# Kernel optimization log

Hardware: AMD Instinct MI355X
Metric: run time of the kernel (lower is better)

## Reference

```python
import jax, jax.numpy as jnp
import numpy as np

B, S, D, H = 4, 1024, 512, 8
DH = D // H  # 64 head dim; max_len == S for the masked (preceding_only) skew path


def setup_inputs() -> dict:
    key = jax.random.key(0)
    ks = jax.random.split(key, 8)
    queries = jax.random.normal(ks[0], (B, S, D), jnp.float32)
    keys_ = jax.random.normal(ks[1], (B, S, D), jnp.float32)
    values = jax.random.normal(ks[2], (B, S, D), jnp.float32)
    Wq = jax.random.normal(ks[3], (D, D), jnp.float32) * 0.03
    Wk = jax.random.normal(ks[4], (D, D), jnp.float32) * 0.03
    Wv = jax.random.normal(ks[5], (D, D), jnp.float32) * 0.03
    Wo = jax.random.normal(ks[6], (D, D), jnp.float32) * 0.03
    rel_emb = jax.random.normal(ks[7], (H, DH, S), jnp.float32) * 0.03  # preceding_only -> len == max_len
    i = jnp.arange(S)
    mask = jnp.where(i[None, :] > i[:, None], -1e9, 0.0).astype(jnp.float32)[None, None]  # [1,1,S,S] causal
    return {"queries": queries, "keys": keys_, "values": values, "mask": mask,
            "Wq": Wq, "Wk": Wk, "Wv": Wv, "Wo": Wo, "rel_emb": rel_emb}


def _skewed_rel_bias(q, rel_emb):
    # q: [B,H,S,DH], rel_emb: [H,DH,L] with L == max_len == S
    b, h, s, _ = q.shape
    L = rel_emb.shape[-1]
    qe = jnp.einsum('bhsd,hdl->bhsl', q, rel_emb)  # [B,H,S,L]
    # _qe_masking: keep qe[..., i, j] where j >= L-1-i
    lengths = (L - 1) - jnp.arange(s)
    keep = (jnp.arange(L)[None, :] >= lengths[:, None]).astype(qe.dtype)
    qe = qe * keep
    # skew: pad one column on the left, fold into [B,H,L+1,S], drop first row
    qe = jnp.pad(qe, ((0, 0), (0, 0), (0, 0), (1, 0)))
    qe = qe.reshape(b, h, L + 1, s)[:, :, 1:, :]  # [B,H,L,S]
    return qe


def reference(queries, keys, values, mask, Wq, Wk, Wv, Wo, rel_emb):
    b, s, _ = queries.shape
    h, dh, _ = rel_emb.shape
    scale = dh ** -0.5

    def split(x):  # [B,S,H*DH] -> [B,H,S,DH]
        return x.reshape(b, s, h, dh).transpose(0, 2, 1, 3)

    q = split(queries @ Wq)
    k = split(keys @ Wk)
    v = split(values @ Wv)

    logits = jnp.einsum('bhsd,bhtd->bhst', q, k)
    logits = logits + _skewed_rel_bias(q, rel_emb)
    logits = (logits + mask[:, :, :s, :s]) * scale  # original scales after adding mask
    weights = jax.nn.softmax(logits, axis=-1)
    ctx = jnp.einsum('bhst,bhtd->bhsd', weights, v)
    ctx = ctx.transpose(0, 2, 1, 3).reshape(b, s, h * dh)
    return ctx @ Wo
```

## Files before the change

kernel.cpp:

```cpp
#include <hip/hip_runtime.h>
#include <hip/hip_bf16.h>

#define SB 4
#define SS 1024
#define SD 512
#define SH 8
#define SDH 64

typedef short bf16x8 __attribute__((ext_vector_type(8)));
typedef float f32x4 __attribute__((ext_vector_type(4)));

#define MFMA(a, b, c) __builtin_amdgcn_mfma_f32_16x16x32_bf16(a, b, c, 0, 0, 0)

__device__ __forceinline__ void load_lds16(const void* g, void* l) {
  __builtin_amdgcn_global_load_lds(
      (__attribute__((address_space(1))) void*)(const_cast<void*>(g)),
      (__attribute__((address_space(3))) void*)(l), 16, 0, 0);
}

__global__ __launch_bounds__(256) void k_prep(
    const float* __restrict__ q, const float* __restrict__ k, const float* __restrict__ v,
    const float* __restrict__ Wq, const float* __restrict__ Wk, const float* __restrict__ Wv,
    const float* __restrict__ Wo, const float* __restrict__ rel,
    __hip_bfloat16* __restrict__ Xq, __hip_bfloat16* __restrict__ Xk,
    __hip_bfloat16* __restrict__ Xv, __hip_bfloat16* __restrict__ Wqt,
    __hip_bfloat16* __restrict__ Wkt, __hip_bfloat16* __restrict__ Wvt,
    __hip_bfloat16* __restrict__ Wot, __hip_bfloat16* __restrict__ relT) {
  __shared__ float tile[32][33];
  const int y = blockIdx.y, x = blockIdx.x, t = threadIdx.x;
  if (y < 3) {
    const float2* in = (const float2*)(y == 0 ? q : y == 1 ? k : v);
    __hip_bfloat162* out = (__hip_bfloat162*)(y == 0 ? Xq : y == 1 ? Xk : Xv);
    const int n2 = SB * SS * SD / 2;
    int i = x * 256 + t, st = 512 * 256;
    for (; i < n2; i += st) out[i] = __float22bfloat162_rn(in[i]);
    return;
  }
  int tx = t & 31, ty = t >> 5;
  if (y < 5) {
    int which = (y - 3) * 2 + (x >> 8), idx = x & 255;
    const float* ip = which == 0 ? Wq : which == 1 ? Wk : which == 2 ? Wv : Wo;
    __hip_bfloat16* op = which == 0 ? Wqt : which == 1 ? Wkt : which == 2 ? Wvt : Wot;
    int c0 = (idx & 15) * 32, r0 = (idx >> 4) * 32;
    for (int rr = ty; rr < 32; rr += 8) tile[rr][tx] = ip[(size_t)(r0 + rr) * SD + c0 + tx];
    __syncthreads();
    for (int cc = ty; cc < 32; cc += 8)
      op[(size_t)(c0 + cc) * SD + r0 + tx] = __float2bfloat16(tile[tx][cc]);
    return;
  }
  int hd = x >> 6, idx = x & 63;
  int c0 = (idx >> 1) * 32, r0 = (idx & 1) * 32;
  const float* ip = rel + (size_t)hd * SDH * SS;
  __hip_bfloat16* op = relT + (size_t)hd * SDH * SS;
  for (int rr = ty; rr < 32; rr += 8) tile[rr][tx] = ip[(size_t)(r0 + rr) * SS + c0 + tx];
  __syncthreads();
  for (int cc = ty; cc < 32; cc += 8)
    op[(size_t)(c0 + cc) * SDH + r0 + tx] = __float2bfloat16(tile[tx][cc]);
}

__device__ __forceinline__ void gemm_core(const __hip_bfloat16* __restrict__ A,
                                          const __hip_bfloat16* __restrict__ Bt,
                                          void* __restrict__ Cout, int mode) {
  __shared__ __hip_bfloat16 As[128 * 64];
  __shared__ __hip_bfloat16 Bs[64 * 64];
  const int t = threadIdx.x, w = t >> 6, lane = t & 63;
  const int quad = lane >> 4, l16 = lane & 15;
  const int m0 = blockIdx.y * 128, n0 = blockIdx.x * 64;
  const int wm = (w >> 1) * 64, wn = (w & 1) * 32;
  f32x4 zero4 = {0.0f, 0.0f, 0.0f, 0.0f};
  f32x4 acc[4][2];
#pragma unroll
  for (int mi = 0; mi < 4; ++mi)
#pragma unroll
    for (int nj = 0; nj < 2; ++nj) acc[mi][nj] = zero4;

  for (int kt = 0; kt < SD; kt += 64) {
#pragma unroll
    for (int c = 0; c < 4; ++c) {
      int ofs = c * 256 + t;
      int row = ofs >> 3, col = (ofs & 7) ^ (row & 7);
      load_lds16(A + (size_t)(m0 + row) * SD + kt + col * 8,
                 (char*)As + (size_t)(c * 256 + w * 64) * 16);
    }
#pragma unroll
    for (int c = 0; c < 2; ++c) {
      int ofs = c * 256 + t;
      int row = ofs >> 3, col = (ofs & 7) ^ (row & 7);
      load_lds16(Bt + (size_t)(n0 + row) * SD + kt + col * 8,
                 (char*)Bs + (size_t)(c * 256 + w * 64) * 16);
    }
    __syncthreads();
    bf16x8 af[4][2], bfr[2][2];
#pragma unroll
    for (int mi = 0; mi < 4; ++mi) {
      int row = wm + mi * 16 + l16;
#pragma unroll
      for (int ks = 0; ks < 2; ++ks)
        af[mi][ks] = *(const bf16x8*)((const char*)As + row * 128 +
                                      ((ks * 4 + quad) ^ (row & 7)) * 16);
    }
#pragma unroll
    for (int nj = 0; nj < 2; ++nj) {
      int row = wn + nj * 16 + l16;
#pragma unroll
      for (int ks = 0; ks < 2; ++ks)
        bfr[nj][ks] = *(const bf16x8*)((const char*)Bs + row * 128 +
                                       ((ks * 4 + quad) ^ (row & 7)) * 16);
    }
#pragma unroll
    for (int mi = 0; mi < 4; ++mi)
#pragma unroll
      for (int nj = 0; nj < 2; ++nj) {
        acc[mi][nj] = MFMA(af[mi][0], bfr[nj][0], acc[mi][nj]);
        acc[mi][nj] = MFMA(af[mi][1], bfr[nj][1], acc[mi][nj]);
      }
    __syncthreads();
  }
#pragma unroll
  for (int mi = 0; mi < 4; ++mi)
#pragma unroll
    for (int nj = 0; nj < 2; ++nj)
#pragma unroll
      for (int r = 0; r < 4; ++r) {
        int m = m0 + wm + mi * 16 + quad * 4 + r;
        int n = n0 + wn + nj * 16 + l16;
        float v = acc[mi][nj][r];
        if (mode == 2) {
          ((float*)Cout)[(size_t)m * SD + n] = v;
        } else {
          int b = m >> 10, s = m & 1023, hh = n >> 6, dh = n & 63;
          __hip_bfloat16 bv = __float2bfloat16(v);
          if (mode == 0)
            ((__hip_bfloat16*)Cout)[((size_t)(b * SH + hh) * SS + s) * SDH + dh] = bv;
          else
            ((__hip_bfloat16*)Cout)[((size_t)(b * SH + hh) * SDH + dh) * SS + s] = bv;
        }
      }
}

__global__ __launch_bounds__(256) void k_gemm_qkv(
    const __hip_bfloat16* __restrict__ Xq, const __hip_bfloat16* __restrict__ Xk,
    const __hip_bfloat16* __restrict__ Xv, const __hip_bfloat16* __restrict__ Wqt,
    const __hip_bfloat16* __restrict__ Wkt, const __hip_bfloat16* __restrict__ Wvt,
    __hip_bfloat16* __restrict__ Qb, __hip_bfloat16* __restrict__ Kb,
    __hip_bfloat16* __restrict__ Vt) {
  int z = blockIdx.z;
  const __hip_bfloat16* A = z == 0 ? Xq : z == 1 ? Xk : Xv;
  const __hip_bfloat16* Bt = z == 0 ? Wqt : z == 1 ? Wkt : Wvt;
  void* C = z == 0 ? (void*)Qb : z == 1 ? (void*)Kb : (void*)Vt;
  gemm_core(A, Bt, C, z == 2 ? 1 : 0);
}

__global__ __launch_bounds__(256) void k_gemm_o(const __hip_bfloat16* __restrict__ CTX,
                                                const __hip_bfloat16* __restrict__ Wot,
                                                float* __restrict__ Out) {
  gemm_core(CTX, Wot, Out, 2);
}

__device__ const int TTm[40] = {0,1,2,3,4,4,5,5,6,6,7,7,8,8,8,9,9,9,10,10,10,11,11,11,
                                12,12,12,12,13,13,13,13,14,14,14,14,15,15,15,15};
__device__ const int CCm[40] = {0,0,0,0,0,1,0,1,0,1,0,1,0,1,2,0,1,2,0,1,2,0,1,2,
                                0,1,2,3,0,1,2,3,0,1,2,3,0,1,2,3};

__global__ __launch_bounds__(256) void k_flash(const __hip_bfloat16* __restrict__ Qb,
                                               const __hip_bfloat16* __restrict__ Kb,
                                               const __hip_bfloat16* __restrict__ Vt,
                                               const __hip_bfloat16* __restrict__ relT,
                                               float* __restrict__ Opart,
                                               float* __restrict__ lpart) {
  __shared__ __hip_bfloat16 Klds[64 * 64];
  __shared__ __hip_bfloat16 Vlds[64 * 64];
  __shared__ __hip_bfloat16 REs[128 * 64];
  __shared__ __hip_bfloat16 QEP[64 * 136];
  const int t = threadIdx.x, w = t >> 6, lane = t & 63;
  const int quad = lane >> 4, l16 = lane & 15;
  const int idx = blockIdx.x, bh = blockIdx.y, h = bh & 7;
  const int tI = TTm[idx], c = CCm[idx];
  const int i0 = tI * 64;
  const int rem = tI + 1 - c * 4;
  const int nt = rem < 4 ? rem : 4;
  const size_t qbase = (size_t)bh * SS * SDH;
  const __hip_bfloat16* Rp = relT + (size_t)h * SS * SDH;

  const int qrow = i0 + w * 16 + l16;
  bf16x8 qf0 = *(const bf16x8*)(Qb + qbase + (size_t)qrow * SDH + quad * 8);
  bf16x8 qf1 = *(const bf16x8*)(Qb + qbase + (size_t)qrow * SDH + 32 + quad * 8);

  f32x4 zero4 = {0.0f, 0.0f, 0.0f, 0.0f};
  f32x4 acc_o[4];
#pragma unroll
  for (int dt = 0; dt < 4; ++dt) acc_o[dt] = zero4;
  float ls[4] = {0.0f, 0.0f, 0.0f, 0.0f};
  const int rloc = quad * 4;
  const int irow_base = i0 + w * 16 + rloc;

  for (int jt = 0; jt < nt; ++jt) {
    const int jtile = c * 4 + jt, j0 = jtile * 64;
    const int l0 = 960 - 64 * (tI - jtile);
#pragma unroll
    for (int cc = 0; cc < 2; ++cc) {
      int ofs = cc * 256 + t;
      int row = ofs >> 3, col = (ofs & 7) ^ (row & 7);
      load_lds16(Kb + qbase + (size_t)(j0 + row) * SDH + col * 8,
                 (char*)Klds + (size_t)(cc * 256 + w * 64) * 16);
      load_lds16(Vt + (size_t)bh * SDH * SS + (size_t)row * SS + j0 + col * 8,
                 (char*)Vlds + (size_t)(cc * 256 + w * 64) * 16);
    }
#pragma unroll
    for (int cc = 0; cc < 4; ++cc) {
      int ofs = cc * 256 + t;
      int row = ofs >> 3, col = (ofs & 7) ^ (row & 7);
      int lr = l0 + row;
      if (lr > 1023) lr = 1023;
      load_lds16(Rp + (size_t)lr * SDH + col * 8,
                 (char*)REs + (size_t)(cc * 256 + w * 64) * 16);
    }
    __syncthreads();

    f32x4 s[4];
#pragma unroll
    for (int nj = 0; nj < 4; ++nj) {
      int row = nj * 16 + l16;
      bf16x8 b0 = *(const bf16x8*)((const char*)Klds + row * 128 + (quad ^ (row & 7)) * 16);
      bf16x8 b1 = *(const bf16x8*)((const char*)Klds + row * 128 + ((4 + quad) ^ (row & 7)) * 16);
      f32x4 z = zero4;
      z = MFMA(qf0, b0, z);
      z = MFMA(qf1, b1, z);
      s[nj] = z;
    }
#pragma unroll
    for (int nc = 0; nc < 8; ++nc) {
      int row = nc * 16 + l16;
      bf16x8 b0 = *(const bf16x8*)((const char*)REs + row * 128 + (quad ^ (row & 7)) * 16);
      bf16x8 b1 = *(const bf16x8*)((const char*)REs + row * 128 + ((4 + quad) ^ (row & 7)) * 16);
      f32x4 e = zero4;
      e = MFMA(qf0, b0, e);
      e = MFMA(qf1, b1, e);
#pragma unroll
      for (int r = 0; r < 4; ++r)
        QEP[(w * 16 + rloc + r) * 136 + nc * 16 + l16] = __float2bfloat16(e[r]);
    }
    __syncthreads();

#pragma unroll
    for (int nj = 0; nj < 4; ++nj) {
      int jc = nj * 16 + l16, jcol = j0 + jc;
#pragma unroll
      for (int r = 0; r < 4; ++r) {
        int il = w * 16 + rloc + r;
        int irow = i0 + il;
        float bias = __bfloat162float(QEP[il * 136 + 63 + jc - (rloc + r)]);
        float val = (s[nj][r] + bias) * 0.125f - 8.0f;
        float p = (jcol <= irow) ? __expf(val) : 0.0f;
        s[nj][r] = p;
        ls[r] += p;
      }
    }
#pragma unroll
    for (int nj = 0; nj < 4; ++nj)
#pragma unroll
      for (int r = 0; r < 4; ++r)
        QEP[(w * 16 + rloc + r) * 136 + nj * 16 + l16] = __float2bfloat16(s[nj][r]);
    __syncthreads();

#pragma unroll
    for (int js = 0; js < 2; ++js) {
      bf16x8 pa = *(const bf16x8*)(QEP + (size_t)(w * 16 + l16) * 136 + js * 32 + quad * 8);
#pragma unroll
      for (int dt = 0; dt < 4; ++dt) {
        int row = dt * 16 + l16;
        bf16x8 vb = *(const bf16x8*)((const char*)Vlds + row * 128 +
                                     ((js * 4 + quad) ^ (row & 7)) * 16);
        acc_o[dt] = MFMA(pa, vb, acc_o[dt]);
      }
    }
    __syncthreads();
  }
  const size_t pbase = (size_t)(bh * 16 + tI) * 4 + c;
  float* Op = Opart + pbase * 4096;
#pragma unroll
  for (int r = 0; r < 4; ++r) {
    float sum = ls[r];
    sum += __shfl_xor(sum, 1, 64);
    sum += __shfl_xor(sum, 2, 64);
    sum += __shfl_xor(sum, 4, 64);
    sum += __shfl_xor(sum, 8, 64);
    int row = w * 16 + rloc + r;
#pragma unroll
    for (int dt = 0; dt < 4; ++dt) Op[row * 64 + dt * 16 + l16] = acc_o[dt][r];
    if (l16 == 0) lpart[pbase * 64 + row] = sum;
  }
}

__global__ __launch_bounds__(256) void k_reduce(const float* __restrict__ Opart,
                                                const float* __restrict__ lpart,
                                                __hip_bfloat16* __restrict__ CTX) {
  const int tI = blockIdx.x, bh = blockIdx.y, b = bh >> 3, h = bh & 7;
  const int nc = tI / 4 + 1;
  const int tid = threadIdx.x;
  __shared__ float lsum[64];
  const size_t base = (size_t)(bh * 16 + tI) * 4;
  if (tid < 64) {
    float s = 0.0f;
    for (int cc = 0; cc < nc; ++cc) s += lpart[(base + cc) * 64 + tid];
    lsum[tid] = s;
  }
  __syncthreads();
  const int e0 = tid * 16;
  const int row = e0 >> 6, d0 = e0 & 63;
  float4 o[4] = {};
  for (int cc = 0; cc < nc; ++cc) {
    const float4* p = (const float4*)(Opart + (base + cc) * 4096);
#pragma unroll
    for (int vv = 0; vv < 4; ++vv) {
      float4 x = p[tid * 4 + vv];
      o[vv].x += x.x; o[vv].y += x.y; o[vv].z += x.z; o[vv].w += x.w;
    }
  }
  const float rl = 1.0f / lsum[row];
  __hip_bfloat16* op = CTX + ((size_t)b * SS + tI * 64 + row) * SD + h * SDH + d0;
#pragma unroll
  for (int vv = 0; vv < 4; ++vv) {
    op[vv * 4 + 0] = __float2bfloat16(o[vv].x * rl);
    op[vv * 4 + 1] = __float2bfloat16(o[vv].y * rl);
    op[vv * 4 + 2] = __float2bfloat16(o[vv].z * rl);
    op[vv * 4 + 3] = __float2bfloat16(o[vv].w * rl);
  }
}

extern "C" void kernel_launch(void* const* d_in, const int* in_sizes, int n_in,
                              void* d_out, int out_size, void* d_ws, size_t ws_size,
                              hipStream_t stream) {
  const float* queries = (const float*)d_in[0];
  const float* keys    = (const float*)d_in[1];
  const float* values  = (const float*)d_in[2];
  const float* Wq = (const float*)d_in[4];
  const float* Wk = (const float*)d_in[5];
  const float* Wv = (const float*)d_in[6];
  const float* Wo = (const float*)d_in[7];
  const float* rel = (const float*)d_in[8];

  char* ws = (char*)d_ws;
  size_t off = 0;
  auto alloc = [&](size_t bytes) {
    char* p = ws + off;
    off += (bytes + 255) & ~(size_t)255;
    return p;
  };
  const size_t XB = (size_t)SB * SS * SD * 2;
  const size_t WB = (size_t)SD * SD * 2;
  __hip_bfloat16* Wqt  = (__hip_bfloat16*)alloc(WB);
  __hip_bfloat16* Wkt  = (__hip_bfloat16*)alloc(WB);
  __hip_bfloat16* Wvt  = (__hip_bfloat16*)alloc(WB);
  __hip_bfloat16* Wot  = (__hip_bfloat16*)alloc(WB);
  __hip_bfloat16* relT = (__hip_bfloat16*)alloc((size_t)SH * SS * SDH * 2);
  __hip_bfloat16* Qb   = (__hip_bfloat16*)alloc(XB);
  __hip_bfloat16* Kb   = (__hip_bfloat16*)alloc(XB);
  __hip_bfloat16* Vt   = (__hip_bfloat16*)alloc(XB);
  __hip_bfloat16* CTX  = (__hip_bfloat16*)alloc(XB);
  char* uni = alloc((size_t)2048 * 4096 * 4 + (size_t)2048 * 64 * 4);
  __hip_bfloat16* Xq = (__hip_bfloat16*)uni;
  __hip_bfloat16* Xk = (__hip_bfloat16*)(uni + XB);
  __hip_bfloat16* Xv = (__hip_bfloat16*)(uni + 2 * XB);
  float* Opart = (float*)uni;
  float* lpart = (float*)(uni + (size_t)2048 * 4096 * 4);
  if (off > ws_size) return;

  k_prep<<<dim3(512, 6), dim3(256), 0, stream>>>(
      queries, keys, values, Wq, Wk, Wv, Wo, rel,
      Xq, Xk, Xv, Wqt, Wkt, Wvt, Wot, relT);
  k_gemm_qkv<<<dim3(SD / 64, SB * SS / 128, 3), dim3(256), 0, stream>>>(
      Xq, Xk, Xv, Wqt, Wkt, Wvt, Qb, Kb, Vt);
  k_flash<<<dim3(40, SB * SH), dim3(256), 0, stream>>>(Qb, Kb, Vt, relT, Opart, lpart);
  k_reduce<<<dim3(16, SB * SH), dim3(256), 0, stream>>>(Opart, lpart, CTX);
  k_gemm_o<<<dim3(SD / 64, SB * SS / 128), dim3(256), 0, stream>>>(CTX, Wot, (float*)d_out);
}
```

Before: 158.7 us.

## Load K, V, rel_emb fragments directly from global and drop block barriers

The flash kernel no longer stages K, V and the relative-embedding tile in shared memory. Each wave now reads its MFMA operands straight from global memory, and the QEP scratch is laid out as per-wave private rows, which removes every __syncthreads in the inner loop. The aim is to cut LDS traffic and barrier stalls. The cost is that all four waves redundantly load the same K/V/rel data from global or L2, with less coalesced 16-byte reads.

```diff
diff --git a/kernel.cpp b/kernel.cpp
--- a/kernel.cpp
+++ b/kernel.cpp
@@ -168,10 +168,7 @@
                                                const __hip_bfloat16* __restrict__ relT,
                                                float* __restrict__ Opart,
                                                float* __restrict__ lpart) {
-  __shared__ __hip_bfloat16 Klds[64 * 64];
-  __shared__ __hip_bfloat16 Vlds[64 * 64];
-  __shared__ __hip_bfloat16 REs[128 * 64];
-  __shared__ __hip_bfloat16 QEP[64 * 136];
+  __shared__ __hip_bfloat16 QEP[64 * 200];
   const int t = threadIdx.x, w = t >> 6, lane = t & 63;
   const int quad = lane >> 4, l16 = lane & 15;
   const int idx = blockIdx.x, bh = blockIdx.y, h = bh & 7;
@@ -180,6 +177,7 @@
   const int rem = tI + 1 - c * 4;
   const int nt = rem < 4 ? rem : 4;
   const size_t qbase = (size_t)bh * SS * SDH;
+  const size_t vbase = (size_t)bh * SDH * SS;
   const __hip_bfloat16* Rp = relT + (size_t)h * SS * SDH;
 
   const int qrow = i0 + w * 16 + l16;
@@ -192,64 +190,46 @@
   for (int dt = 0; dt < 4; ++dt) acc_o[dt] = zero4;
   float ls[4] = {0.0f, 0.0f, 0.0f, 0.0f};
   const int rloc = quad * 4;
-  const int irow_base = i0 + w * 16 + rloc;
+  __hip_bfloat16* myrow = QEP + (size_t)(w * 16 + rloc) * 200;
 
   for (int jt = 0; jt < nt; ++jt) {
     const int jtile = c * 4 + jt, j0 = jtile * 64;
     const int l0 = 960 - 64 * (tI - jtile);
-#pragma unroll
-    for (int cc = 0; cc < 2; ++cc) {
-      int ofs = cc * 256 + t;
-      int row = ofs >> 3, col = (ofs & 7) ^ (row & 7);
-      load_lds16(Kb + qbase + (size_t)(j0 + row) * SDH + col * 8,
-                 (char*)Klds + (size_t)(cc * 256 + w * 64) * 16);
-      load_lds16(Vt + (size_t)bh * SDH * SS + (size_t)row * SS + j0 + col * 8,
-                 (char*)Vlds + (size_t)(cc * 256 + w * 64) * 16);
-    }
-#pragma unroll
-    for (int cc = 0; cc < 4; ++cc) {
-      int ofs = cc * 256 + t;
-      int row = ofs >> 3, col = (ofs & 7) ^ (row & 7);
-      int lr = l0 + row;
-      if (lr > 1023) lr = 1023;
-      load_lds16(Rp + (size_t)lr * SDH + col * 8,
-                 (char*)REs + (size_t)(cc * 256 + w * 64) * 16);
-    }
-    __syncthreads();
+
+#pragma unroll
+    for (int nc = 0; nc < 8; ++nc) {
+      int l = l0 + nc * 16 + l16;
+      if (l > 1023) l = 1023;
+      const __hip_bfloat16* rp = Rp + (size_t)l * SDH;
+      bf16x8 rb0 = *(const bf16x8*)(rp + quad * 8);
+      bf16x8 rb1 = *(const bf16x8*)(rp + 32 + quad * 8);
+      f32x4 e = zero4;
+      e = MFMA(qf0, rb0, e);
+      e = MFMA(qf1, rb1, e);
+#pragma unroll
+      for (int r = 0; r < 4; ++r)
+        myrow[r * 200 + nc * 16 + l16] = __float2bfloat16(e[r]);
+    }
 
     f32x4 s[4];
 #pragma unroll
     for (int nj = 0; nj < 4; ++nj) {
-      int row = nj * 16 + l16;
-      bf16x8 b0 = *(const bf16x8*)((const char*)Klds + row * 128 + (quad ^ (row & 7)) * 16);
-      bf16x8 b1 = *(const bf16x8*)((const char*)Klds + row * 128 + ((4 + quad) ^ (row & 7)) * 16);
+      const __hip_bfloat16* kp = Kb + qbase + (size_t)(j0 + nj * 16 + l16) * SDH;
+      bf16x8 kb0 = *(const bf16x8*)(kp + quad * 8);
+      bf16x8 kb1 = *(const bf16x8*)(kp + 32 + quad * 8);
       f32x4 z = zero4;
-      z = MFMA(qf0, b0, z);
-      z = MFMA(qf1, b1, z);
+      z = MFMA(qf0, kb0, z);
+      z = MFMA(qf1, kb1, z);
       s[nj] = z;
     }
-#pragma unroll
-    for (int nc = 0; nc < 8; ++nc) {
-      int row = nc * 16 + l16;
-      bf16x8 b0 = *(const bf16x8*)((const char*)REs + row * 128 + (quad ^ (row & 7)) * 16);
-      bf16x8 b1 = *(const bf16x8*)((const char*)REs + row * 128 + ((4 + quad) ^ (row & 7)) * 16);
-      f32x4 e = zero4;
-      e = MFMA(qf0, b0, e);
-      e = MFMA(qf1, b1, e);
-#pragma unroll
-      for (int r = 0; r < 4; ++r)
-        QEP[(w * 16 + rloc + r) * 136 + nc * 16 + l16] = __float2bfloat16(e[r]);
-    }
-    __syncthreads();
 
 #pragma unroll
     for (int nj = 0; nj < 4; ++nj) {
       int jc = nj * 16 + l16, jcol = j0 + jc;
 #pragma unroll
       for (int r = 0; r < 4; ++r) {
-        int il = w * 16 + rloc + r;
-        int irow = i0 + il;
-        float bias = __bfloat162float(QEP[il * 136 + 63 + jc - (rloc + r)]);
+        int irow = i0 + w * 16 + rloc + r;
+        float bias = __bfloat162float(myrow[r * 200 + 63 + jc - (rloc + r)]);
         float val = (s[nj][r] + bias) * 0.125f - 8.0f;
         float p = (jcol <= irow) ? __expf(val) : 0.0f;
         s[nj][r] = p;
@@ -260,21 +240,20 @@
     for (int nj = 0; nj < 4; ++nj)
 #pragma unroll
       for (int r = 0; r < 4; ++r)
-        QEP[(w * 16 + rloc + r) * 136 + nj * 16 + l16] = __float2bfloat16(s[nj][r]);
-    __syncthreads();
+        myrow[r * 200 + 128 + nj * 16 + l16] = __float2bfloat16(s[nj][r]);
 
 #pragma unroll
     for (int js = 0; js < 2; ++js) {
-      bf16x8 pa = *(const bf16x8*)(QEP + (size_t)(w * 16 + l16) * 136 + js * 32 + quad * 8);
+      bf16x8 pa = *(const bf16x8*)(QEP + (size_t)(w * 16 + l16) * 200 + 128 +
+                                   js * 32 + quad * 8);
 #pragma unroll
       for (int dt = 0; dt < 4; ++dt) {
-        int row = dt * 16 + l16;
-        bf16x8 vb = *(const bf16x8*)((const char*)Vlds + row * 128 +
-                                     ((js * 4 + quad) ^ (row & 7)) * 16);
+        const __hip_bfloat16* vp =
+            Vt + vbase + (size_t)(dt * 16 + l16) * SS + j0 + js * 32 + quad * 8;
+        bf16x8 vb = *(const bf16x8*)vp;
         acc_o[dt] = MFMA(pa, vb, acc_o[dt]);
       }
     }
-    __syncthreads();
   }
   const size_t pbase = (size_t)(bh * 16 + tI) * 4 + c;
   float* Op = Opart + pbase * 4096;
```

After: 197.0 us. +24.1%, slower.
